# Kernel optimization log

Hardware: AMD Instinct MI355X
Metric: run time of the kernel (lower is better)

The kernel has to match this reference:

```python
import jax, jax.numpy as jnp
import numpy as np

N_NODES = 100000
N_EDGES = 1280000
IN_DIM = 64
HID = 64
OUT_DIM = 2
N_GRAPHS = 1000
BN_EPS = 1e-5


def setup_inputs() -> dict:
    key = jax.random.key(0)
    ks = jax.random.split(key, 16)
    x = jax.random.normal(ks[0], (N_NODES, IN_DIM), dtype=jnp.float32)
    edge_index = jax.random.randint(ks[1], (2, N_EDGES), 0, N_NODES, dtype=jnp.int64)
    batch = jnp.sort(jax.random.randint(ks[2], (N_NODES,), 0, N_GRAPHS, dtype=jnp.int64))
    # He-init linear weights (stored as [in, out] so forward is x @ W)
    def he(k, fan_in, fan_out):
        return jax.random.normal(k, (fan_in, fan_out), dtype=jnp.float32) * np.sqrt(2.0 / fan_in)
    return {
        "x": x,
        "edge_index": edge_index,
        "batch": batch,
        "bn_in_g": jnp.ones((IN_DIM,), jnp.float32),
        "bn_in_b": jnp.zeros((IN_DIM,), jnp.float32),
        "W1": he(ks[3], IN_DIM, HID), "b1": jnp.zeros((HID,), jnp.float32),
        "g1": jnp.ones((HID,), jnp.float32), "be1": jnp.zeros((HID,), jnp.float32),
        "W2": he(ks[4], HID, HID), "b2": jnp.zeros((HID,), jnp.float32),
        "g2": jnp.ones((HID,), jnp.float32), "be2": jnp.zeros((HID,), jnp.float32),
        "Wout": he(ks[5], HID, OUT_DIM), "bout": jnp.zeros((OUT_DIM,), jnp.float32),
    }


def _batchnorm(x, g, b):
    # training-mode BN over the node dimension (biased variance, as torch uses for normalization)
    m = jnp.mean(x, axis=0)
    v = jnp.mean(jnp.square(x - m), axis=0)
    return (x - m) * jax.lax.rsqrt(v + BN_EPS) * g + b


def _gcn_norm(edge_index, n):
    # PyG GCNConv normalization with added self-loops:
    # norm_e = deg[src]^-1/2 * deg[dst]^-1/2, deg computed on A + I over targets.
    row = jnp.concatenate([edge_index[0], jnp.arange(n, dtype=edge_index.dtype)])
    col = jnp.concatenate([edge_index[1], jnp.arange(n, dtype=edge_index.dtype)])
    deg = jax.ops.segment_sum(jnp.ones_like(col, dtype=jnp.float32), col, num_segments=n)
    dinv = jnp.where(deg > 0, jax.lax.rsqrt(deg), 0.0)
    norm = dinv[row] * dinv[col]
    return row, col, norm


def _gcn_conv(x, W, b, row, col, norm, n):
    h = x @ W                                   # [N, out]
    msg = h[row] * norm[:, None]                # gather over edges (incl. self-loops)
    agg = jax.ops.segment_sum(msg, col, num_segments=n)
    return agg + b


def reference(x, edge_index, batch, bn_in_g, bn_in_b, W1, b1, g1, be1, W2, b2, g2, be2, Wout, bout):
    n = x.shape[0]
    row, col, norm = _gcn_norm(edge_index, n)
    h = _batchnorm(x, bn_in_g, bn_in_b)         # input BN (dropout = identity in eval)
    h = _gcn_conv(h, W1, b1, row, col, norm, n)
    h = _batchnorm(jax.nn.relu(h), g1, be1)
    h = _gcn_conv(h, W2, b2, row, col, norm, n)
    h = _batchnorm(jax.nn.relu(h), g2, be2)
    # global mean pool per graph
    sums = jax.ops.segment_sum(h, batch, num_segments=N_GRAPHS)
    cnts = jax.ops.segment_sum(jnp.ones((n,), h.dtype), batch, num_segments=N_GRAPHS)
    pooled = sums / jnp.maximum(cnts, 1.0)[:, None]
    return pooled @ Wout + bout                 # [N_GRAPHS, OUT_DIM]
```

## Files before the change

kernel.cpp:

```cpp
#include <hip/hip_runtime.h>
#include <math.h>

#define N_NODES 100000
#define N_EDGES 1280000
#define DIM 64
#define N_GRAPHS 1000
#define BN_EPS 1e-5f
#define NB 392
#define P1B 256
#define P1E 5000
#define SB 400
#define WIN 128
#define NWIN (N_EDGES / WIN)
#define GU 8
#define NSLOT 32

__device__ __forceinline__ unsigned int bf16_rtn2(float a, float b) {
    unsigned int ua = __float_as_uint(a);
    unsigned int ub = __float_as_uint(b);
    ua = (ua + 0x7FFFu + ((ua >> 16) & 1u)) >> 16;
    ub = (ub + 0x7FFFu + ((ub >> 16) & 1u)) >> 16;
    return ua | (ub << 16);
}
__device__ __forceinline__ unsigned short bf16r(float a) {
    unsigned int u = __float_as_uint(a);
    return (unsigned short)((u + 0x7FFFu + ((u >> 16) & 1u)) >> 16);
}
__device__ __forceinline__ float bfup(unsigned short u) {
    return __uint_as_float(((unsigned int)u) << 16);
}

__global__ __launch_bounds__(256) void k_p1hist(const int* __restrict__ ei,
                                                const int* __restrict__ batch,
                                                const float* __restrict__ X,
                                                int* __restrict__ bh,
                                                int* __restrict__ start,
                                                float* __restrict__ gsum,
                                                float* __restrict__ gsumsq) {
    int t = threadIdx.x;
    if (blockIdx.x < P1B) {
        __shared__ int hist[NB];
        for (int b = t; b < NB; b += 256) hist[b] = 0;
        __syncthreads();
        int e0 = blockIdx.x * P1E;
        #pragma unroll 4
        for (int e = e0 + t; e < e0 + P1E; e += 256)
            atomicAdd(&hist[ei[N_EDGES + e] >> 8], 1);
        __syncthreads();
        for (int b = t; b < NB; b += 256) bh[b * P1B + blockIdx.x] = hist[b];
    } else if (blockIdx.x < P1B + SB) {
        int grp = blockIdx.x - P1B;
        int j = t & 63, rg = t >> 6;
        int base = grp * 250;
        float s = 0.f, s2 = 0.f;
        for (int i = base + rg; i < base + 250; i += 4) {
            float v = X[i * DIM + j];
            s += v; s2 += v * v;
        }
        __shared__ float ls[256], ls2[256];
        ls[t] = s; ls2[t] = s2;
        __syncthreads();
        if (t < 64) {
            int slot = (grp & (NSLOT - 1)) * DIM;
            s  = ls[j]  + ls[64 + j]  + ls[128 + j]  + ls[192 + j];
            s2 = ls2[j] + ls2[64 + j] + ls2[128 + j] + ls2[192 + j];
            atomicAdd(&gsum[slot + j], s);
            atomicAdd(&gsumsq[slot + j], s2);
        }
    } else {
        int i = (blockIdx.x - P1B - SB) * 256 + t;
        if (i < N_NODES) {
            int cur = batch[i];
            if (i == 0) { for (int q = 0; q <= cur; q++) start[q] = 0; }
            else {
                int prev = batch[i - 1];
                for (int q = prev + 1; q <= cur; q++) start[q] = i;
            }
            if (i == N_NODES - 1)
                for (int q = cur + 1; q <= N_GRAPHS; q++) start[q] = N_NODES;
        }
    }
}

__global__ void k_scan1(const int* __restrict__ bh, int* __restrict__ iscan,
                        int* __restrict__ bsum) {
    __shared__ int ls[256];
    int i = blockIdx.x * 256 + threadIdx.x;
    int v = bh[i];
    ls[threadIdx.x] = v;
    __syncthreads();
    for (int off = 1; off < 256; off <<= 1) {
        int tv = (threadIdx.x >= off) ? ls[threadIdx.x - off] : 0;
        __syncthreads();
        ls[threadIdx.x] += tv;
        __syncthreads();
    }
    iscan[i] = ls[threadIdx.x];
    if (threadIdx.x == 255) bsum[blockIdx.x] = ls[255];
}

__global__ void k_scan2(const int* __restrict__ bsum, int* __restrict__ boff) {
    __shared__ int ls[512];
    int t = threadIdx.x;
    int v0 = (t < NB) ? bsum[t] : 0;
    ls[t] = v0;
    __syncthreads();
    for (int off = 1; off < 512; off <<= 1) {
        int v = (t >= off) ? ls[t - off] : 0;
        __syncthreads();
        ls[t] += v;
        __syncthreads();
    }
    if (t < NB) boff[t] = ls[t] - v0;
}

__global__ __launch_bounds__(256) void k_p1scat(const int* __restrict__ ei,
                                                const int* __restrict__ bh,
                                                const int* __restrict__ iscan,
                                                const int* __restrict__ boff,
                                                int2* __restrict__ tmp) {
    __shared__ int cur[NB];
    int blk = blockIdx.x;
    for (int b = threadIdx.x; b < NB; b += 256) {
        int i = b * P1B + blk;
        cur[b] = boff[b] + iscan[i] - bh[i];
    }
    __syncthreads();
    int e0 = blk * P1E;
    for (int e = e0 + threadIdx.x; e < e0 + P1E; e += 256) {
        int r = ei[e], c = ei[N_EDGES + e];
        int pos = atomicAdd(&cur[c >> 8], 1);
        tmp[pos] = make_int2(r, c);
    }
}

__global__ __launch_bounds__(256) void k_p2a(const int2* __restrict__ tmp,
                                             const int* __restrict__ bh,
                                             const int* __restrict__ iscan,
                                             const int* __restrict__ boff,
                                             int* __restrict__ rowstart,
                                             float* __restrict__ dinv,
                                             int* __restrict__ winnode) {
    int b = blockIdx.x, t = threadIdx.x;
    int bstart = boff[b] + iscan[b * 256] - bh[b * 256];
    int bend = (b == NB - 1) ? N_EDGES
                             : (boff[b + 1] + iscan[(b + 1) * 256] - bh[(b + 1) * 256]);
    __shared__ int cnt[256], scn[256];
    cnt[t] = 0;
    __syncthreads();
    for (int e = bstart + t; e < bend; e += 256)
        atomicAdd(&cnt[tmp[e].y & 255], 1);
    __syncthreads();
    scn[t] = cnt[t];
    __syncthreads();
    for (int off = 1; off < 256; off <<= 1) {
        int v = (t >= off) ? scn[t - off] : 0;
        __syncthreads();
        scn[t] += v;
        __syncthreads();
    }
    int node = b * 256 + t;
    int rs = bstart + scn[t] - cnt[t];
    if (node <= N_NODES) rowstart[node] = rs;
    if (node < N_NODES) {
        int deg = cnt[t];
        dinv[node] = 1.0f / sqrtf((float)(deg + 1));
        int re = rs + deg;
        for (int w = (rs + WIN - 1) / WIN; w * WIN < re; ++w) winnode[w] = node;
    }
}

__global__ __launch_bounds__(256) void k_p2b(const int2* __restrict__ tmp,
                                             const int* __restrict__ bh,
                                             const int* __restrict__ iscan,
                                             const int* __restrict__ boff,
                                             const int* __restrict__ rowstart,
                                             const float* __restrict__ dinv,
                                             int2* __restrict__ csr_ew) {
    int b = blockIdx.x, t = threadIdx.x;
    int bstart = boff[b] + iscan[b * 256] - bh[b * 256];
    int bend = (b == NB - 1) ? N_EDGES
                             : (boff[b + 1] + iscan[(b + 1) * 256] - bh[(b + 1) * 256]);
    __shared__ int curs[256];
    __shared__ float dl[256];
    int node = b * 256 + t;
    curs[t] = (node < N_NODES) ? rowstart[node] : 0;
    dl[t]   = (node < N_NODES) ? dinv[node] : 0.f;
    __syncthreads();
    for (int e = bstart + t; e < bend; e += 256) {
        int2 rec = tmp[e];
        int ld = rec.y & 255;
        int pos = atomicAdd(&curs[ld], 1);
        float w = dl[ld] * dinv[rec.x];
        csr_ew[pos] = make_int2(rec.x, (int)__float_as_uint(w));
    }
}

__global__ void k_bnfold(float* __restrict__ gsum, float* __restrict__ gsumsq,
                         const float* __restrict__ g, const float* __restrict__ b,
                         const float* __restrict__ W,
                         float* __restrict__ scale, float* __restrict__ cshift) {
    int j = threadIdx.x;
    float ms = 0.f, m2 = 0.f;
    for (int k = 0; k < NSLOT; k++) {
        ms += gsum[k * DIM + j];   gsum[k * DIM + j] = 0.f;
        m2 += gsumsq[k * DIM + j]; gsumsq[k * DIM + j] = 0.f;
    }
    float mean = ms * (1.0f / N_NODES);
    float var  = m2 * (1.0f / N_NODES) - mean * mean;
    float inv  = 1.0f / sqrtf(var + BN_EPS);
    float sc   = g[j] * inv;
    scale[j] = sc;
    __shared__ float shl[64];
    shl[j] = b[j] - mean * sc;
    __syncthreads();
    float s = 0.f;
    for (int k = 0; k < DIM; k++) s += shl[k] * W[k * DIM + j];
    cshift[j] = s;
}

__global__ void k_bnfinal(const float* __restrict__ gsum, const float* __restrict__ gsumsq,
                          const float* __restrict__ g, const float* __restrict__ b,
                          float* __restrict__ scale, float* __restrict__ shift) {
    int j = threadIdx.x;
    float ms = 0.f, m2 = 0.f;
    for (int k = 0; k < NSLOT; k++) { ms += gsum[k * DIM + j]; m2 += gsumsq[k * DIM + j]; }
    float mean = ms * (1.0f / N_NODES);
    float var  = m2 * (1.0f / N_NODES) - mean * mean;
    float inv  = 1.0f / sqrtf(var + BN_EPS);
    float sc   = g[j] * inv;
    scale[j] = sc;
    shift[j] = b[j] - mean * sc;
}

__global__ __launch_bounds__(256) void k_gemm_f32(const float* __restrict__ X,
                                                  const float* __restrict__ W,
                                                  const float* __restrict__ scale,
                                                  const float* __restrict__ cshift,
                                                  unsigned short* __restrict__ T) {
    __shared__ float Wl[64 * 64];
    __shared__ float Al[64 * 65];
    for (int t = threadIdx.x; t < 4096; t += 256) {
        int k = t >> 6;
        Wl[t] = W[t] * scale[k];
    }
    int row0 = blockIdx.x * 64;
    for (int t = threadIdx.x; t < 4096; t += 256) {
        int r = t >> 6, k = t & 63;
        int i = row0 + r;
        Al[r * 65 + k] = (i < N_NODES) ? X[(size_t)i * DIM + k] : 0.f;
    }
    __syncthreads();
    int r = threadIdx.x & 63;
    int q = threadIdx.x >> 6;
    float acc[16];
    #pragma unroll
    for (int jj = 0; jj < 16; jj++) acc[jj] = cshift[q * 16 + jj];
    #pragma unroll 4
    for (int k = 0; k < 64; k++) {
        float a = Al[r * 65 + k];
        const float4* wv = (const float4*)&Wl[k * 64 + q * 16];
        float4 w0 = wv[0], w1 = wv[1], w2 = wv[2], w3 = wv[3];
        acc[0]  += a * w0.x; acc[1]  += a * w0.y; acc[2]  += a * w0.z; acc[3]  += a * w0.w;
        acc[4]  += a * w1.x; acc[5]  += a * w1.y; acc[6]  += a * w1.z; acc[7]  += a * w1.w;
        acc[8]  += a * w2.x; acc[9]  += a * w2.y; acc[10] += a * w2.z; acc[11] += a * w2.w;
        acc[12] += a * w3.x; acc[13] += a * w3.y; acc[14] += a * w3.z; acc[15] += a * w3.w;
    }
    int i = row0 + r;
    if (i < N_NODES) {
        unsigned int pk[8];
        #pragma unroll
        for (int jj = 0; jj < 8; jj++) pk[jj] = bf16_rtn2(acc[2 * jj], acc[2 * jj + 1]);
        uint4* outv = (uint4*)&T[(size_t)i * DIM + q * 16];
        outv[0] = make_uint4(pk[0], pk[1], pk[2], pk[3]);
        outv[1] = make_uint4(pk[4], pk[5], pk[6], pk[7]);
    }
}

__global__ __launch_bounds__(256) void k_gemm_b16(const unsigned short* __restrict__ X,
                                                  const float* __restrict__ W,
                                                  const float* __restrict__ scale,
                                                  const float* __restrict__ cshift,
                                                  unsigned short* __restrict__ T) {
    __shared__ float Wl[64 * 64];
    __shared__ float Al[64 * 65];
    for (int t = threadIdx.x; t < 4096; t += 256) {
        int k = t >> 6;
        Wl[t] = W[t] * scale[k];
    }
    int row0 = blockIdx.x * 64;
    for (int t = threadIdx.x; t < 4096; t += 256) {
        int r = t >> 6, k = t & 63;
        int i = row0 + r;
        Al[r * 65 + k] = (i < N_NODES) ? bfup(X[(size_t)i * DIM + k]) : 0.f;
    }
    __syncthreads();
    int r = threadIdx.x & 63;
    int q = threadIdx.x >> 6;
    float acc[16];
    #pragma unroll
    for (int jj = 0; jj < 16; jj++) acc[jj] = cshift[q * 16 + jj];
    #pragma unroll 4
    for (int k = 0; k < 64; k++) {
        float a = Al[r * 65 + k];
        const float4* wv = (const float4*)&Wl[k * 64 + q * 16];
        float4 w0 = wv[0], w1 = wv[1], w2 = wv[2], w3 = wv[3];
        acc[0]  += a * w0.x; acc[1]  += a * w0.y; acc[2]  += a * w0.z; acc[3]  += a * w0.w;
        acc[4]  += a * w1.x; acc[5]  += a * w1.y; acc[6]  += a * w1.z; acc[7]  += a * w1.w;
        acc[8]  += a * w2.x; acc[9]  += a * w2.y; acc[10] += a * w2.z; acc[11] += a * w2.w;
        acc[12] += a * w3.x; acc[13] += a * w3.y; acc[14] += a * w3.z; acc[15] += a * w3.w;
    }
    int i = row0 + r;
    if (i < N_NODES) {
        unsigned int pk[8];
        #pragma unroll
        for (int jj = 0; jj < 8; jj++) pk[jj] = bf16_rtn2(acc[2 * jj], acc[2 * jj + 1]);
        uint4* outv = (uint4*)&T[(size_t)i * DIM + q * 16];
        outv[0] = make_uint4(pk[0], pk[1], pk[2], pk[3]);
        outv[1] = make_uint4(pk[4], pk[5], pk[6], pk[7]);
    }
}

__global__ __launch_bounds__(256) void k_zstrad(const int* __restrict__ rowstart,
                                                const int* __restrict__ winnode,
                                                float* __restrict__ C) {
    int lane = threadIdx.x & 63;
    int w = blockIdx.x * 4 + (threadIdx.x >> 6);
    int n = winnode[w];
    if (rowstart[n] < w * WIN)
        C[(size_t)n * DIM + lane] = 0.f;
}

__global__ __launch_bounds__(256) void k_gather1(const unsigned short* __restrict__ T,
                                                 const float* __restrict__ dinv,
                                                 const int* __restrict__ rowstart,
                                                 const int* __restrict__ winnode,
                                                 const int2* __restrict__ csr_ew,
                                                 const float* __restrict__ bias,
                                                 float* __restrict__ C,
                                                 unsigned short* __restrict__ H,
                                                 float* __restrict__ gsum,
                                                 float* __restrict__ gsumsq) {
    int lane = threadIdx.x & 63;
    int w = blockIdx.x * 4 + (threadIdx.x >> 6);
    float bb = bias[lane];
    float s = 0.f, s2 = 0.f;
    int e = w * WIN;
    const int eend = e + WIN;
    int i  = __builtin_amdgcn_readfirstlane(winnode[w]);
    int re = __builtin_amdgcn_readfirstlane(rowstart[i + 1]);
    bool part = __builtin_amdgcn_readfirstlane(rowstart[i]) < e;
    float acc = 0.f;
    for (; e < eend; e += GU) {
        int src[GU]; float wt[GU];
        int eu = __builtin_amdgcn_readfirstlane(e);
        #pragma unroll
        for (int u = 0; u < GU; u++) {
            int2 ew = csr_ew[eu + u];
            src[u] = ew.x; wt[u] = __uint_as_float((unsigned int)ew.y);
        }
        float tv[GU];
        #pragma unroll
        for (int u = 0; u < GU; u++) tv[u] = bfup(T[(size_t)src[u] * DIM + lane]);
        #pragma unroll
        for (int u = 0; u < GU; u++) {
            while (e + u == re) {
                if (part) { atomicAdd(&C[(size_t)i * DIM + lane], acc); part = false; }
                else {
                    float di = dinv[i];
                    float h = fmaxf(acc + bfup(T[(size_t)i * DIM + lane]) * (di * di) + bb, 0.f);
                    H[(size_t)i * DIM + lane] = bf16r(h);
                    s += h; s2 += h * h;
                }
                acc = 0.f; ++i;
                re = __builtin_amdgcn_readfirstlane(rowstart[i + 1]);
            }
            acc += tv[u] * wt[u];
        }
    }
    if (part || re > eend) atomicAdd(&C[(size_t)i * DIM + lane], acc);
    else {
        float di = dinv[i];
        float h = fmaxf(acc + bfup(T[(size_t)i * DIM + lane]) * (di * di) + bb, 0.f);
        H[(size_t)i * DIM + lane] = bf16r(h);
        s += h; s2 += h * h;
    }
    __shared__ float ls[256], ls2[256];
    ls[threadIdx.x] = s; ls2[threadIdx.x] = s2;
    __syncthreads();
    if (threadIdx.x < 64) {
        int j = threadIdx.x;
        int slot = (blockIdx.x & (NSLOT - 1)) * DIM;
        atomicAdd(&gsum[slot + j],   ls[j] + ls[64 + j] + ls[128 + j] + ls[192 + j]);
        atomicAdd(&gsumsq[slot + j], ls2[j] + ls2[64 + j] + ls2[128 + j] + ls2[192 + j]);
    }
}

__global__ __launch_bounds__(256) void k_gather2(const unsigned short* __restrict__ T,
                                                 const float* __restrict__ dinv,
                                                 const int* __restrict__ rowstart,
                                                 const int* __restrict__ winnode,
                                                 const int2* __restrict__ csr_ew,
                                                 const float* __restrict__ bias,
                                                 const int* __restrict__ batch,
                                                 float* __restrict__ C,
                                                 float* __restrict__ pool,
                                                 float* __restrict__ gsum,
                                                 float* __restrict__ gsumsq) {
    int lane = threadIdx.x & 63;
    int w = blockIdx.x * 4 + (threadIdx.x >> 6);
    float bb = bias[lane];
    float s = 0.f, s2 = 0.f, ps = 0.f;
    int cur_g = -1;
    int e = w * WIN;
    const int eend = e + WIN;
    int i  = __builtin_amdgcn_readfirstlane(winnode[w]);
    int re = __builtin_amdgcn_readfirstlane(rowstart[i + 1]);
    bool part = __builtin_amdgcn_readfirstlane(rowstart[i]) < e;
    float acc = 0.f;
    for (; e < eend; e += GU) {
        int src[GU]; float wt[GU];
        int eu = __builtin_amdgcn_readfirstlane(e);
        #pragma unroll
        for (int u = 0; u < GU; u++) {
            int2 ew = csr_ew[eu + u];
            src[u] = ew.x; wt[u] = __uint_as_float((unsigned int)ew.y);
        }
        float tv[GU];
        #pragma unroll
        for (int u = 0; u < GU; u++) tv[u] = bfup(T[(size_t)src[u] * DIM + lane]);
        #pragma unroll
        for (int u = 0; u < GU; u++) {
            while (e + u == re) {
                if (part) { atomicAdd(&C[(size_t)i * DIM + lane], acc); part = false; }
                else {
                    float di = dinv[i];
                    float h = fmaxf(acc + bfup(T[(size_t)i * DIM + lane]) * (di * di) + bb, 0.f);
                    s += h; s2 += h * h;
                    int g = batch[i];
                    if (g != cur_g) {
                        if (cur_g >= 0) atomicAdd(&pool[(size_t)cur_g * DIM + lane], ps);
                        ps = 0.f; cur_g = g;
                    }
                    ps += h;
                }
                acc = 0.f; ++i;
                re = __builtin_amdgcn_readfirstlane(rowstart[i + 1]);
            }
            acc += tv[u] * wt[u];
        }
    }
    if (part || re > eend) atomicAdd(&C[(size_t)i * DIM + lane], acc);
    else {
        float di = dinv[i];
        float h = fmaxf(acc + bfup(T[(size_t)i * DIM + lane]) * (di * di) + bb, 0.f);
        s += h; s2 += h * h;
        int g = batch[i];
        if (g != cur_g) {
            if (cur_g >= 0) atomicAdd(&pool[(size_t)cur_g * DIM + lane], ps);
            ps = 0.f; cur_g = g;
        }
        ps += h;
    }
    if (cur_g >= 0) atomicAdd(&pool[(size_t)cur_g * DIM + lane], ps);
    __shared__ float ls[256], ls2[256];
    ls[threadIdx.x] = s; ls2[threadIdx.x] = s2;
    __syncthreads();
    if (threadIdx.x < 64) {
        int j = threadIdx.x;
        int slot = (blockIdx.x & (NSLOT - 1)) * DIM;
        atomicAdd(&gsum[slot + j],   ls[j] + ls[64 + j] + ls[128 + j] + ls[192 + j]);
        atomicAdd(&gsumsq[slot + j], ls2[j] + ls2[64 + j] + ls2[128 + j] + ls2[192 + j]);
    }
}

__global__ __launch_bounds__(256) void k_strad1(const float* __restrict__ C,
                                                const unsigned short* __restrict__ T,
                                                const float* __restrict__ dinv,
                                                const int* __restrict__ rowstart,
                                                const int* __restrict__ winnode,
                                                const float* __restrict__ bias,
                                                unsigned short* __restrict__ H,
                                                float* __restrict__ gsum,
                                                float* __restrict__ gsumsq) {
    int lane = threadIdx.x & 63;
    int wv = threadIdx.x >> 6;
    float bb = bias[lane];
    float s = 0.f, s2 = 0.f;
    __shared__ int anyw;
    if (threadIdx.x == 0) anyw = 0;
    __syncthreads();
    if (blockIdx.x < NWIN / 4) {
        int w = blockIdx.x * 4 + wv;
        int n = winnode[w];
        int rs = rowstart[n];
        if (w == rs / WIN + 1) {
            float di = dinv[n];
            float h = fmaxf(C[(size_t)n * DIM + lane]
                            + bfup(T[(size_t)n * DIM + lane]) * (di * di) + bb, 0.f);
            H[(size_t)n * DIM + lane] = bf16r(h);
            s += h; s2 += h * h;
            anyw = 1;
        }
    } else {
        int base = (blockIdx.x - NWIN / 4) * 256 + wv * 64;
        int nb = base + lane;
        int d0 = 0;
        if (nb < N_NODES)
            d0 = (rowstart[nb + 1] == rowstart[nb]) && ((rowstart[nb] & (WIN - 1)) == 0);
        unsigned long long m = __ballot(d0);
        while (m) {
            int b = __builtin_ctzll(m);
            m &= m - 1;
            int n = base + b;
            float di = dinv[n];
            float h = fmaxf(bfup(T[(size_t)n * DIM + lane]) * (di * di) + bb, 0.f);
            H[(size_t)n * DIM + lane] = bf16r(h);
            s += h; s2 += h * h;
            anyw = 1;
        }
    }
    __shared__ float ls[256], ls2[256];
    ls[threadIdx.x] = s; ls2[threadIdx.x] = s2;
    __syncthreads();
    if (anyw && threadIdx.x < 64) {
        int j = threadIdx.x;
        int slot = (blockIdx.x & (NSLOT - 1)) * DIM;
        atomicAdd(&gsum[slot + j],   ls[j] + ls[64 + j] + ls[128 + j] + ls[192 + j]);
        atomicAdd(&gsumsq[slot + j], ls2[j] + ls2[64 + j] + ls2[128 + j] + ls2[192 + j]);
    }
}

__global__ __launch_bounds__(256) void k_strad2(const float* __restrict__ C,
                                                const unsigned short* __restrict__ T,
                                                const float* __restrict__ dinv,
                                                const int* __restrict__ rowstart,
                                                const int* __restrict__ winnode,
                                                const float* __restrict__ bias,
                                                const int* __restrict__ batch,
                                                float* __restrict__ pool,
                                                float* __restrict__ gsum,
                                                float* __restrict__ gsumsq) {
    int lane = threadIdx.x & 63;
    int wv = threadIdx.x >> 6;
    float bb = bias[lane];
    float s = 0.f, s2 = 0.f;
    __shared__ int anyw;
    if (threadIdx.x == 0) anyw = 0;
    __syncthreads();
    if (blockIdx.x < NWIN / 4) {
        int w = blockIdx.x * 4 + wv;
        int n = winnode[w];
        int rs = rowstart[n];
        if (w == rs / WIN + 1) {
            float di = dinv[n];
            float h = fmaxf(C[(size_t)n * DIM + lane]
                            + bfup(T[(size_t)n * DIM + lane]) * (di * di) + bb, 0.f);
            s += h; s2 += h * h;
            atomicAdd(&pool[(size_t)batch[n] * DIM + lane], h);
            anyw = 1;
        }
    } else {
        int base = (blockIdx.x - NWIN / 4) * 256 + wv * 64;
        int nb = base + lane;
        int d0 = 0;
        if (nb < N_NODES)
            d0 = (rowstart[nb + 1] == rowstart[nb]) && ((rowstart[nb] & (WIN - 1)) == 0);
        unsigned long long m = __ballot(d0);
        while (m) {
            int b = __builtin_ctzll(m);
            m &= m - 1;
            int n = base + b;
            float di = dinv[n];
            float h = fmaxf(bfup(T[(size_t)n * DIM + lane]) * (di * di) + bb, 0.f);
            s += h; s2 += h * h;
            atomicAdd(&pool[(size_t)batch[n] * DIM + lane], h);
            anyw = 1;
        }
    }
    __shared__ float ls[256], ls2[256];
    ls[threadIdx.x] = s; ls2[threadIdx.x] = s2;
    __syncthreads();
    if (anyw && threadIdx.x < 64) {
        int j = threadIdx.x;
        int slot = (blockIdx.x & (NSLOT - 1)) * DIM;
        atomicAdd(&gsum[slot + j],   ls[j] + ls[64 + j] + ls[128 + j] + ls[192 + j]);
        atomicAdd(&gsumsq[slot + j], ls2[j] + ls2[64 + j] + ls2[128 + j] + ls2[192 + j]);
    }
}

__global__ void k_final(const float* __restrict__ pool, const int* __restrict__ start,
                        const float* __restrict__ scale, const float* __restrict__ shift,
                        const float* __restrict__ Wout, const float* __restrict__ bout,
                        float* __restrict__ out) {
    int g = blockIdx.x;
    int l = threadIdx.x;
    float c = fmaxf((float)(start[g + 1] - start[g]), 1.f);
    float p = (pool[g * DIM + l] / c) * scale[l] + shift[l];
    float a0 = p * Wout[l * 2 + 0];
    float a1 = p * Wout[l * 2 + 1];
    #pragma unroll
    for (int off = 32; off; off >>= 1) {
        a0 += __shfl_down(a0, off, 64);
        a1 += __shfl_down(a1, off, 64);
    }
    if (l == 0) {
        out[g * 2 + 0] = a0 + bout[0];
        out[g * 2 + 1] = a1 + bout[1];
    }
}

extern "C" void kernel_launch(void* const* d_in, const int* in_sizes, int n_in,
                              void* d_out, int out_size, void* d_ws, size_t ws_size,
                              hipStream_t stream) {
    (void)in_sizes; (void)n_in; (void)out_size; (void)ws_size;
    const float* x       = (const float*)d_in[0];
    const int*   ei      = (const int*)d_in[1];
    const int*   batch   = (const int*)d_in[2];
    const float* bn_in_g = (const float*)d_in[3];
    const float* bn_in_b = (const float*)d_in[4];
    const float* W1      = (const float*)d_in[5];
    const float* b1      = (const float*)d_in[6];
    const float* g1      = (const float*)d_in[7];
    const float* be1     = (const float*)d_in[8];
    const float* W2      = (const float*)d_in[9];
    const float* b2      = (const float*)d_in[10];
    const float* g2      = (const float*)d_in[11];
    const float* be2     = (const float*)d_in[12];
    const float* Wout    = (const float*)d_in[13];
    const float* bout    = (const float*)d_in[14];
    float* out = (float*)d_out;

    char* p = (char*)d_ws;
    float* C = (float*)p;                   p += (size_t)N_NODES * DIM * 4;
    unsigned short* H = (unsigned short*)p; p += (size_t)N_NODES * DIM * 2;
    unsigned short* T = (unsigned short*)p; p += (size_t)N_NODES * DIM * 2;
    int2* csr_ew = (int2*)p;                p += (size_t)N_EDGES * 8;
    float* dinv = (float*)p;                p += N_NODES * 4;
    int* bh = (int*)p;                      p += NB * P1B * 4;
    int* iscan = (int*)p;                   p += NB * P1B * 4;
    int* rowstart = (int*)p;                p += (N_NODES + 2) * 4;
    int* winnode = (int*)p;                 p += NWIN * 4;
    int* bsum = (int*)p;                    p += NB * 4;
    int* boff = (int*)p;                    p += NB * 4;
    int* start = (int*)p;                   p += (N_GRAPHS + 2) * 4;
    float* gsum = (float*)p;                p += NSLOT * DIM * 4;
    float* gsumsq = (float*)p;              p += NSLOT * DIM * 4;
    float* scale = (float*)p;               p += DIM * 4;
    float* shift = (float*)p;               p += DIM * 4;
    float* cshift = (float*)p;              p += DIM * 4;
    float* pool = (float*)p;                p += (size_t)N_GRAPHS * DIM * 4;
    int2* tmp = (int2*)H;

    hipMemsetAsync(gsum, 0, 2 * NSLOT * DIM * sizeof(float), stream);
    hipMemsetAsync(pool, 0, (size_t)N_GRAPHS * DIM * sizeof(float), stream);
    k_p1hist<<<P1B + SB + 392, 256, 0, stream>>>(ei, batch, x, bh, start, gsum, gsumsq);
    k_scan1<<<NB, 256, 0, stream>>>(bh, iscan, bsum);
    k_scan2<<<1, 512, 0, stream>>>(bsum, boff);
    k_p1scat<<<P1B, 256, 0, stream>>>(ei, bh, iscan, boff, tmp);
    k_p2a<<<NB, 256, 0, stream>>>(tmp, bh, iscan, boff, rowstart, dinv, winnode);
    k_p2b<<<NB, 256, 0, stream>>>(tmp, bh, iscan, boff, rowstart, dinv, csr_ew);

    k_bnfold<<<1, 64, 0, stream>>>(gsum, gsumsq, bn_in_g, bn_in_b, W1, scale, cshift);
    k_gemm_f32<<<(N_NODES + 63) / 64, 256, 0, stream>>>(x, W1, scale, cshift, T);
    k_zstrad<<<NWIN / 4, 256, 0, stream>>>(rowstart, winnode, C);
    k_gather1<<<NWIN / 4, 256, 0, stream>>>(T, dinv, rowstart, winnode, csr_ew, b1,
                                            C, H, gsum, gsumsq);
    k_strad1<<<NWIN / 4 + 392, 256, 0, stream>>>(C, T, dinv, rowstart, winnode, b1,
                                                 H, gsum, gsumsq);

    k_bnfold<<<1, 64, 0, stream>>>(gsum, gsumsq, g1, be1, W2, scale, cshift);
    k_gemm_b16<<<(N_NODES + 63) / 64, 256, 0, stream>>>(H, W2, scale, cshift, T);
    k_zstrad<<<NWIN / 4, 256, 0, stream>>>(rowstart, winnode, C);
    k_gather2<<<NWIN / 4, 256, 0, stream>>>(T, dinv, rowstart, winnode, csr_ew, b2,
                                            batch, C, pool, gsum, gsumsq);
    k_strad2<<<NWIN / 4 + 392, 256, 0, stream>>>(C, T, dinv, rowstart, winnode, b2,
                                                 batch, pool, gsum, gsumsq);

    k_bnfinal<<<1, 64, 0, stream>>>(gsum, gsumsq, g2, be2, scale, shift);
    k_final<<<N_GRAPHS, 64, 0, stream>>>(pool, start, scale, shift, Wout, bout, out);
}
```

Measured before the change: 353.4 us.

## Fold GCN source normalization into GEMM output, drop per-edge weights from CSR

Scales each transformed row by dinv[src] inside the GEMM epilogue and applies dinv[dst] once after aggregation, so the CSR stores only source indices instead of (index, weight) pairs. This halves the edge-list bytes read in both gather passes and removes the per-edge multiply and the weight computation in the CSR build. The trade-off is that T is rounded to bf16 after the dinv scaling, which changes rounding slightly, and every consumer (gather, straddle, self-loop paths) had to be rewritten to match the new factorization.

```diff
diff --git a/kernel.cpp b/kernel.cpp
--- a/kernel.cpp
+++ b/kernel.cpp
@@ -175,24 +175,19 @@
                                              const int* __restrict__ iscan,
                                              const int* __restrict__ boff,
                                              const int* __restrict__ rowstart,
-                                             const float* __restrict__ dinv,
-                                             int2* __restrict__ csr_ew) {
+                                             int* __restrict__ csr) {
     int b = blockIdx.x, t = threadIdx.x;
     int bstart = boff[b] + iscan[b * 256] - bh[b * 256];
     int bend = (b == NB - 1) ? N_EDGES
                              : (boff[b + 1] + iscan[(b + 1) * 256] - bh[(b + 1) * 256]);
     __shared__ int curs[256];
-    __shared__ float dl[256];
     int node = b * 256 + t;
     curs[t] = (node < N_NODES) ? rowstart[node] : 0;
-    dl[t]   = (node < N_NODES) ? dinv[node] : 0.f;
     __syncthreads();
     for (int e = bstart + t; e < bend; e += 256) {
         int2 rec = tmp[e];
-        int ld = rec.y & 255;
-        int pos = atomicAdd(&curs[ld], 1);
-        float w = dl[ld] * dinv[rec.x];
-        csr_ew[pos] = make_int2(rec.x, (int)__float_as_uint(w));
+        int pos = atomicAdd(&curs[rec.y & 255], 1);
+        csr[pos] = rec.x;
     }
 }
 
@@ -237,13 +232,11 @@
                                                   const float* __restrict__ W,
                                                   const float* __restrict__ scale,
                                                   const float* __restrict__ cshift,
+                                                  const float* __restrict__ dinv,
                                                   unsigned short* __restrict__ T) {
     __shared__ float Wl[64 * 64];
     __shared__ float Al[64 * 65];
-    for (int t = threadIdx.x; t < 4096; t += 256) {
-        int k = t >> 6;
-        Wl[t] = W[t] * scale[k];
-    }
+    for (int t = threadIdx.x; t < 4096; t += 256) Wl[t] = W[t] * scale[t >> 6];
     int row0 = blockIdx.x * 64;
     for (int t = threadIdx.x; t < 4096; t += 256) {
         int r = t >> 6, k = t & 63;
@@ -268,9 +261,11 @@
     }
     int i = row0 + r;
     if (i < N_NODES) {
+        float dv = dinv[i];
         unsigned int pk[8];
         #pragma unroll
-        for (int jj = 0; jj < 8; jj++) pk[jj] = bf16_rtn2(acc[2 * jj], acc[2 * jj + 1]);
+        for (int jj = 0; jj < 8; jj++)
+            pk[jj] = bf16_rtn2(acc[2 * jj] * dv, acc[2 * jj + 1] * dv);
         uint4* outv = (uint4*)&T[(size_t)i * DIM + q * 16];
         outv[0] = make_uint4(pk[0], pk[1], pk[2], pk[3]);
         outv[1] = make_uint4(pk[4], pk[5], pk[6], pk[7]);
@@ -281,13 +276,11 @@
                                                   const float* __restrict__ W,
                                                   const float* __restrict__ scale,
                                                   const float* __restrict__ cshift,
+                                                  const float* __restrict__ dinv,
                                                   unsigned short* __restrict__ T) {
     __shared__ float Wl[64 * 64];
     __shared__ float Al[64 * 65];
-    for (int t = threadIdx.x; t < 4096; t += 256) {
-        int k = t >> 6;
-        Wl[t] = W[t] * scale[k];
-    }
+    for (int t = threadIdx.x; t < 4096; t += 256) Wl[t] = W[t] * scale[t >> 6];
     int row0 = blockIdx.x * 64;
     for (int t = threadIdx.x; t < 4096; t += 256) {
         int r = t >> 6, k = t & 63;
@@ -312,9 +305,11 @@
     }
     int i = row0 + r;
     if (i < N_NODES) {
+        float dv = dinv[i];
         unsigned int pk[8];
         #pragma unroll
-        for (int jj = 0; jj < 8; jj++) pk[jj] = bf16_rtn2(acc[2 * jj], acc[2 * jj + 1]);
+        for (int jj = 0; jj < 8; jj++)
+            pk[jj] = bf16_rtn2(acc[2 * jj] * dv, acc[2 * jj + 1] * dv);
         uint4* outv = (uint4*)&T[(size_t)i * DIM + q * 16];
         outv[0] = make_uint4(pk[0], pk[1], pk[2], pk[3]);
         outv[1] = make_uint4(pk[4], pk[5], pk[6], pk[7]);
@@ -335,7 +330,7 @@
                                                  const float* __restrict__ dinv,
                                                  const int* __restrict__ rowstart,
                                                  const int* __restrict__ winnode,
-                                                 const int2* __restrict__ csr_ew,
+                                                 const int* __restrict__ csr,
                                                  const float* __restrict__ bias,
                                                  float* __restrict__ C,
                                                  unsigned short* __restrict__ H,
@@ -352,13 +347,10 @@
     bool part = __builtin_amdgcn_readfirstlane(rowstart[i]) < e;
     float acc = 0.f;
     for (; e < eend; e += GU) {
-        int src[GU]; float wt[GU];
+        int src[GU];
         int eu = __builtin_amdgcn_readfirstlane(e);
         #pragma unroll
-        for (int u = 0; u < GU; u++) {
-            int2 ew = csr_ew[eu + u];
-            src[u] = ew.x; wt[u] = __uint_as_float((unsigned int)ew.y);
-        }
+        for (int u = 0; u < GU; u++) src[u] = csr[eu + u];
         float tv[GU];
         #pragma unroll
         for (int u = 0; u < GU; u++) tv[u] = bfup(T[(size_t)src[u] * DIM + lane]);
@@ -368,20 +360,20 @@
                 if (part) { atomicAdd(&C[(size_t)i * DIM + lane], acc); part = false; }
                 else {
                     float di = dinv[i];
-                    float h = fmaxf(acc + bfup(T[(size_t)i * DIM + lane]) * (di * di) + bb, 0.f);
+                    float h = fmaxf((acc + bfup(T[(size_t)i * DIM + lane])) * di + bb, 0.f);
                     H[(size_t)i * DIM + lane] = bf16r(h);
                     s += h; s2 += h * h;
                 }
                 acc = 0.f; ++i;
                 re = __builtin_amdgcn_readfirstlane(rowstart[i + 1]);
             }
-            acc += tv[u] * wt[u];
+            acc += tv[u];
         }
     }
     if (part || re > eend) atomicAdd(&C[(size_t)i * DIM + lane], acc);
     else {
         float di = dinv[i];
-        float h = fmaxf(acc + bfup(T[(size_t)i * DIM + lane]) * (di * di) + bb, 0.f);
+        float h = fmaxf((acc + bfup(T[(size_t)i * DIM + lane])) * di + bb, 0.f);
         H[(size_t)i * DIM + lane] = bf16r(h);
         s += h; s2 += h * h;
     }
@@ -400,7 +392,7 @@
                                                  const float* __restrict__ dinv,
                                                  const int* __restrict__ rowstart,
                                                  const int* __restrict__ winnode,
-                                                 const int2* __restrict__ csr_ew,
+                                                 const int* __restrict__ csr,
                                                  const float* __restrict__ bias,
                                                  const int* __restrict__ batch,
                                                  float* __restrict__ C,
@@ -419,13 +411,10 @@
     bool part = __builtin_amdgcn_readfirstlane(rowstart[i]) < e;
     float acc = 0.f;
     for (; e < eend; e += GU) {
-        int src[GU]; float wt[GU];
+        int src[GU];
         int eu = __builtin_amdgcn_readfirstlane(e);
         #pragma unroll
-        for (int u = 0; u < GU; u++) {
-            int2 ew = csr_ew[eu + u];
-            src[u] = ew.x; wt[u] = __uint_as_float((unsigned int)ew.y);
-        }
+        for (int u = 0; u < GU; u++) src[u] = csr[eu + u];
         float tv[GU];
         #pragma unroll
         for (int u = 0; u < GU; u++) tv[u] = bfup(T[(size_t)src[u] * DIM + lane]);
@@ -435,7 +424,7 @@
                 if (part) { atomicAdd(&C[(size_t)i * DIM + lane], acc); part = false; }
                 else {
                     float di = dinv[i];
-                    float h = fmaxf(acc + bfup(T[(size_t)i * DIM + lane]) * (di * di) + bb, 0.f);
+                    float h = fmaxf((acc + bfup(T[(size_t)i * DIM + lane])) * di + bb, 0.f);
                     s += h; s2 += h * h;
                     int g = batch[i];
                     if (g != cur_g) {
@@ -447,13 +436,13 @@
                 acc = 0.f; ++i;
                 re = __builtin_amdgcn_readfirstlane(rowstart[i + 1]);
             }
-            acc += tv[u] * wt[u];
+            acc += tv[u];
         }
     }
     if (part || re > eend) atomicAdd(&C[(size_t)i * DIM + lane], acc);
     else {
         float di = dinv[i];
-        float h = fmaxf(acc + bfup(T[(size_t)i * DIM + lane]) * (di * di) + bb, 0.f);
+        float h = fmaxf((acc + bfup(T[(size_t)i * DIM + lane])) * di + bb, 0.f);
         s += h; s2 += h * h;
         int g = batch[i];
         if (g != cur_g) {
@@ -496,8 +485,8 @@
         int rs = rowstart[n];
         if (w == rs / WIN + 1) {
             float di = dinv[n];
-            float h = fmaxf(C[(size_t)n * DIM + lane]
-                            + bfup(T[(size_t)n * DIM + lane]) * (di * di) + bb, 0.f);
+            float h = fmaxf((C[(size_t)n * DIM + lane]
+                             + bfup(T[(size_t)n * DIM + lane])) * di + bb, 0.f);
             H[(size_t)n * DIM + lane] = bf16r(h);
             s += h; s2 += h * h;
             anyw = 1;
@@ -514,7 +503,7 @@
             m &= m - 1;
             int n = base + b;
             float di = dinv[n];
-            float h = fmaxf(bfup(T[(size_t)n * DIM + lane]) * (di * di) + bb, 0.f);
+            float h = fmaxf(bfup(T[(size_t)n * DIM + lane]) * di + bb, 0.f);
             H[(size_t)n * DIM + lane] = bf16r(h);
             s += h; s2 += h * h;
             anyw = 1;
@@ -554,8 +543,8 @@
         int rs = rowstart[n];
         if (w == rs / WIN + 1) {
             float di = dinv[n];
-            float h = fmaxf(C[(size_t)n * DIM + lane]
-                            + bfup(T[(size_t)n * DIM + lane]) * (di * di) + bb, 0.f);
+            float h = fmaxf((C[(size_t)n * DIM + lane]
+                             + bfup(T[(size_t)n * DIM + lane])) * di + bb, 0.f);
             s += h; s2 += h * h;
             atomicAdd(&pool[(size_t)batch[n] * DIM + lane], h);
             anyw = 1;
@@ -572,7 +561,7 @@
             m &= m - 1;
             int n = base + b;
             float di = dinv[n];
-            float h = fmaxf(bfup(T[(size_t)n * DIM + lane]) * (di * di) + bb, 0.f);
+            float h = fmaxf(bfup(T[(size_t)n * DIM + lane]) * di + bb, 0.f);
             s += h; s2 += h * h;
             atomicAdd(&pool[(size_t)batch[n] * DIM + lane], h);
             anyw = 1;
@@ -635,7 +624,7 @@
     float* C = (float*)p;                   p += (size_t)N_NODES * DIM * 4;
     unsigned short* H = (unsigned short*)p; p += (size_t)N_NODES * DIM * 2;
     unsigned short* T = (unsigned short*)p; p += (size_t)N_NODES * DIM * 2;
-    int2* csr_ew = (int2*)p;                p += (size_t)N_EDGES * 8;
+    int* csr = (int*)p;                     p += (size_t)N_EDGES * 4;
     float* dinv = (float*)p;                p += N_NODES * 4;
     int* bh = (int*)p;                      p += NB * P1B * 4;
     int* iscan = (int*)p;                   p += NB * P1B * 4;
@@ -659,20 +648,20 @@
     k_scan2<<<1, 512, 0, stream>>>(bsum, boff);
     k_p1scat<<<P1B, 256, 0, stream>>>(ei, bh, iscan, boff, tmp);
     k_p2a<<<NB, 256, 0, stream>>>(tmp, bh, iscan, boff, rowstart, dinv, winnode);
-    k_p2b<<<NB, 256, 0, stream>>>(tmp, bh, iscan, boff, rowstart, dinv, csr_ew);
+    k_p2b<<<NB, 256, 0, stream>>>(tmp, bh, iscan, boff, rowstart, csr);
 
     k_bnfold<<<1, 64, 0, stream>>>(gsum, gsumsq, bn_in_g, bn_in_b, W1, scale, cshift);
-    k_gemm_f32<<<(N_NODES + 63) / 64, 256, 0, stream>>>(x, W1, scale, cshift, T);
+    k_gemm_f32<<<(N_NODES + 63) / 64, 256, 0, stream>>>(x, W1, scale, cshift, dinv, T);
     k_zstrad<<<NWIN / 4, 256, 0, stream>>>(rowstart, winnode, C);
-    k_gather1<<<NWIN / 4, 256, 0, stream>>>(T, dinv, rowstart, winnode, csr_ew, b1,
+    k_gather1<<<NWIN / 4, 256, 0, stream>>>(T, dinv, rowstart, winnode, csr, b1,
                                             C, H, gsum, gsumsq);
     k_strad1<<<NWIN / 4 + 392, 256, 0, stream>>>(C, T, dinv, rowstart, winnode, b1,
                                                  H, gsum, gsumsq);
 
     k_bnfold<<<1, 64, 0, stream>>>(gsum, gsumsq, g1, be1, W2, scale, cshift);
-    k_gemm_b16<<<(N_NODES + 63) / 64, 256, 0, stream>>>(H, W2, scale, cshift, T);
+    k_gemm_b16<<<(N_NODES + 63) / 64, 256, 0, stream>>>(H, W2, scale, cshift, dinv, T);
     k_zstrad<<<NWIN / 4, 256, 0, stream>>>(rowstart, winnode, C);
-    k_gather2<<<NWIN / 4, 256, 0, stream>>>(T, dinv, rowstart, winnode, csr_ew, b2,
+    k_gather2<<<NWIN / 4, 256, 0, stream>>>(T, dinv, rowstart, winnode, csr, b2,
                                             batch, C, pool, gsum, gsumsq);
     k_strad2<<<NWIN / 4 + 392, 256, 0, stream>>>(C, T, dinv, rowstart, winnode, b2,
                                                  batch, pool, gsum, gsumsq);
```

After: 335.1 us. 1.05x faster.
